# Performance work log

Measured on AMD Instinct MI355X. Metric: run time of the kernel, lower is better.

## Reference

```python
import jax, jax.numpy as jnp
import numpy as np

N_NODES = 50000
N_EDGES = 1600000
NODE_DIM = 1024
HID = 128
OUT = 128
LN_EPS = 1e-5


def setup_inputs() -> dict:
    key = jax.random.key(0)
    ks = jax.random.split(key, 8)
    s = lambda d: 1.0 / np.sqrt(d)
    return {
        "x": jax.random.normal(ks[0], (N_NODES, NODE_DIM), jnp.float32),
        "edge_index": jax.random.randint(ks[1], (2, N_EDGES), 0, N_NODES, jnp.int64),
        "proj_w": jax.random.normal(ks[2], (HID, NODE_DIM), jnp.float32) * s(NODE_DIM),
        "proj_b": jnp.zeros((HID,), jnp.float32),
        "lin_l_w": jax.random.normal(ks[3], (HID, HID), jnp.float32) * s(HID),
        "lin_l_b": jnp.zeros((HID,), jnp.float32),
        "lin_r_w": jax.random.normal(ks[4], (HID, HID), jnp.float32) * s(HID),
        "ln_g": jnp.ones((HID,), jnp.float32),
        "ln_b": jnp.zeros((HID,), jnp.float32),
        "out_w": jax.random.normal(ks[5], (OUT, HID), jnp.float32) * s(HID),
        "out_b": jnp.zeros((OUT,), jnp.float32),
    }


def reference(x, edge_index, proj_w, proj_b, lin_l_w, lin_l_b, lin_r_w, ln_g, ln_b, out_w, out_b):
    n = x.shape[0]
    # input projection + ReLU: [N, node_dim] -> [N, H]
    h = jax.nn.relu(x @ proj_w.T + proj_b)
    # SAGEConv(mean): gather source features, mean-scatter to targets
    src, dst = edge_index[0], edge_index[1]
    agg = jax.ops.segment_sum(h[src], dst, num_segments=n)  # [N, H]
    deg = jax.ops.segment_sum(jnp.ones((src.shape[0],), h.dtype), dst, num_segments=n)
    mean_nbr = agg / jnp.maximum(deg, 1.0)[:, None]
    h = mean_nbr @ lin_l_w.T + lin_l_b + h @ lin_r_w.T
    # LayerNorm over feature dim
    mu = h.mean(-1, keepdims=True)
    var = jnp.mean((h - mu) ** 2, -1, keepdims=True)
    h = (h - mu) * jax.lax.rsqrt(var + LN_EPS) * ln_g + ln_b
    h = jax.nn.relu(h)  # dropout is identity in eval
    # batch=None -> global mean pool over all nodes: [1, H]
    g = h.mean(0, keepdims=True)
    return g @ out_w.T + out_b
```

## Files before the change

### kernel.cpp

```cpp
#include <hip/hip_runtime.h>

#define N_NODES  50000
#define N_EDGES  1600000
#define NODE_DIM 1024
#define HID      128
#define LN_EPS   1e-5f
#define NBUCK    196
#define SHARD    6250

typedef float f32x4 __attribute__((ext_vector_type(4)));
typedef __bf16 bf16x8 __attribute__((ext_vector_type(8)));
typedef unsigned short u16x8 __attribute__((ext_vector_type(8)));

__device__ __forceinline__ unsigned short f2bf(float f) {
  __bf16 b = (__bf16)f;
  return __builtin_bit_cast(unsigned short, b);
}
__device__ __forceinline__ unsigned int pkbf(float a, float b) {
  return (unsigned int)f2bf(a) | ((unsigned int)f2bf(b) << 16);
}
__device__ __forceinline__ float bf2f(unsigned short v) {
  return __uint_as_float((unsigned int)v << 16);
}

__device__ __forceinline__ int scan256_excl(int v, int buf[2][256], int t) {
  int cur = 0;
  buf[0][t] = v;
  __syncthreads();
  for (int off = 1; off < 256; off <<= 1) {
    int nxt = cur ^ 1;
    int s = buf[cur][t];
    if (t >= off) s += buf[cur][t - off];
    buf[nxt][t] = s;
    cur = nxt;
    __syncthreads();
  }
  return buf[cur][t] - v;
}

__global__ __launch_bounds__(256) void k_wcvt(const float* __restrict__ w,
                                              unsigned short* __restrict__ wb) {
  int i = (blockIdx.x * 256 + threadIdx.x) * 4;
  float4 v = *(const float4*)(w + i);
  unsigned int* o = (unsigned int*)(wb + i);
  o[0] = pkbf(v.x, v.y);
  o[1] = pkbf(v.z, v.w);
}

#define LDR 40

__global__ __launch_bounds__(256) void k_proj(const float* __restrict__ x,
                                              const unsigned short* __restrict__ pwb,
                                              const float* __restrict__ pb,
                                              unsigned short* __restrict__ h) {
  __shared__ unsigned short As[2 * 64 * LDR];
  __shared__ unsigned short Bs[2 * 128 * LDR];
  const int tid = threadIdx.x;
  const int m0 = blockIdx.x * 64;
  const int wave = tid >> 6, lane = tid & 63;
  const int wm = (wave >> 1) * 32, wn = (wave & 1) * 64;
  const int fr = lane & 15, ko = (lane >> 4) * 8;

  const int arow = tid >> 2, akq = (tid & 3) * 16;
  const int grow = m0 + arow;
  const bool aval = (grow < N_NODES);
  const float* aptr = x + (size_t)grow * NODE_DIM + akq;
  const int brow = tid >> 1, bkq = (tid & 1) * 32;
  const unsigned short* bptr = pwb + (size_t)brow * NODE_DIM + bkq;

  f32x4 acc[2][4] = {};
  float4 av[4];
  u16x8 bv[4];

  auto LOAD = [&](int k0) {
    if (aval) {
      const float4* p = (const float4*)(aptr + k0);
#pragma unroll
      for (int j = 0; j < 4; j++) av[j] = p[j];
    } else {
#pragma unroll
      for (int j = 0; j < 4; j++) av[j] = make_float4(0.f, 0.f, 0.f, 0.f);
    }
    const u16x8* q = (const u16x8*)(bptr + k0);
#pragma unroll
    for (int j = 0; j < 4; j++) bv[j] = q[j];
  };

  LOAD(0);
  for (int k0 = 0; k0 < NODE_DIM; k0 += 64) {
    __syncthreads();
    unsigned int* da = (unsigned int*)&As[((akq >> 5) * 64 + arow) * LDR + (akq & 31)];
#pragma unroll
    for (int j = 0; j < 4; j++) {
      da[2 * j]     = pkbf(av[j].x, av[j].y);
      da[2 * j + 1] = pkbf(av[j].z, av[j].w);
    }
    u16x8* db = (u16x8*)&Bs[((bkq >> 5) * 128 + brow) * LDR];
#pragma unroll
    for (int j = 0; j < 4; j++) db[j] = bv[j];
    __syncthreads();

    if (k0 + 64 < NODE_DIM) LOAD(k0 + 64);

#pragma unroll
    for (int s = 0; s < 2; s++) {
      bf16x8 af[2], bfr[4];
#pragma unroll
      for (int m = 0; m < 2; m++)
        af[m] = *(const bf16x8*)&As[(s * 64 + wm + m * 16 + fr) * LDR + ko];
#pragma unroll
      for (int n = 0; n < 4; n++)
        bfr[n] = *(const bf16x8*)&Bs[(s * 128 + wn + n * 16 + fr) * LDR + ko];
#pragma unroll
      for (int m = 0; m < 2; m++)
#pragma unroll
        for (int n = 0; n < 4; n++)
          acc[m][n] = __builtin_amdgcn_mfma_f32_16x16x32_bf16(af[m], bfr[n], acc[m][n], 0, 0, 0);
    }
  }

  const int cr = (lane >> 4) * 4, cc = lane & 15;
#pragma unroll
  for (int n = 0; n < 4; n++) {
    const int col = wn + n * 16 + cc;
    const float bias = pb[col];
#pragma unroll
    for (int m = 0; m < 2; m++) {
#pragma unroll
      for (int i = 0; i < 4; i++) {
        const int row = m0 + wm + m * 16 + cr + i;
        if (row < N_NODES) {
          float v = acc[m][n][i] + bias;
          h[(size_t)row * HID + col] = f2bf(v > 0.f ? v : 0.f);
        }
      }
    }
  }
}

__global__ __launch_bounds__(256) void k_hist(const int* __restrict__ ei,
                                              int* __restrict__ counts) {
  __shared__ int bins[NBUCK];
  int t = threadIdx.x;
  if (t < NBUCK) bins[t] = 0;
  __syncthreads();
  int base = blockIdx.x * SHARD;
  for (int i = t; i < SHARD; i += 256)
    atomicAdd(&bins[ei[N_EDGES + base + i] >> 8], 1);
  __syncthreads();
  if (t < NBUCK) counts[t * 256 + blockIdx.x] = bins[t];
}

__global__ __launch_bounds__(256) void k_s1(const int* __restrict__ counts,
                                            int* __restrict__ basem,
                                            int* __restrict__ btot) {
  __shared__ int buf[2][256];
  int t = threadIdx.x, b = blockIdx.x;
  int v = counts[b * 256 + t];
  int excl = scan256_excl(v, buf, t);
  basem[b * 256 + t] = excl;
  if (t == 255) btot[b] = excl + v;
}

__global__ __launch_bounds__(256) void k_s2(const int* __restrict__ btot,
                                            int* __restrict__ bstart,
                                            float* __restrict__ accum) {
  __shared__ int buf[2][256];
  int t = threadIdx.x;
  int v = (t < NBUCK) ? btot[t] : 0;
  int excl = scan256_excl(v, buf, t);
  if (t < NBUCK) bstart[t] = excl;
  if (t == 0) bstart[NBUCK] = N_EDGES;
  if (t < HID) accum[t] = 0.f;
}

__global__ __launch_bounds__(256) void k_scatter(const int* __restrict__ ei,
                                                 const int* __restrict__ basem,
                                                 const int* __restrict__ bstart,
                                                 unsigned int* __restrict__ bs) {
  __shared__ int cur[NBUCK];
  int t = threadIdx.x;
  if (t < NBUCK) cur[t] = bstart[t] + basem[t * 256 + blockIdx.x];
  __syncthreads();
  int base = blockIdx.x * SHARD;
  for (int i = t; i < SHARD; i += 256) {
    int e = base + i;
    unsigned int src = (unsigned int)ei[e];
    unsigned int dst = (unsigned int)ei[N_EDGES + e];
    int pos = atomicAdd(&cur[dst >> 8], 1);
    bs[pos] = src | ((dst & 255u) << 16);
  }
}

__global__ __launch_bounds__(256) void k_bucket(const int* __restrict__ bstart,
                                                const unsigned int* __restrict__ bs,
                                                unsigned short* __restrict__ nbr,
                                                int* __restrict__ offs,
                                                int* __restrict__ deg) {
  __shared__ int bins[256];
  __shared__ int buf[2][256];
  __shared__ int curs[256];
  int t = threadIdx.x, b = blockIdx.x;
  int s = bstart[b], e = bstart[b + 1];
  bins[t] = 0;
  __syncthreads();
  for (int i = s + t; i < e; i += 256)
    atomicAdd(&bins[(bs[i] >> 16) & 255u], 1);
  __syncthreads();
  int v = bins[t];
  int excl = scan256_excl(v, buf, t);
  int node = b * 256 + t;
  deg[node]  = v;
  offs[node] = s + excl;
  curs[t]    = s + excl;
  __syncthreads();
  for (int i = s + t; i < e; i += 256) {
    unsigned int p = bs[i];
    int pos = atomicAdd(&curs[(p >> 16) & 255u], 1);
    nbr[pos] = (unsigned short)(p & 0xffffu);
  }
}

__global__ __launch_bounds__(256) void k_gather(const unsigned short* __restrict__ h,
                                                const unsigned short* __restrict__ nbr,
                                                const int* __restrict__ offs,
                                                const int* __restrict__ deg,
                                                unsigned short* __restrict__ mn) {
  const int wave = threadIdx.x >> 6;
  const int lane = threadIdx.x & 63;
  const int node = blockIdx.x * 4 + wave;
  if (node >= N_NODES) return;
  const int g = lane >> 4, li = lane & 15;
  const int d  = deg[node];
  const int st = offs[node];
  float a[8] = {0.f, 0.f, 0.f, 0.f, 0.f, 0.f, 0.f, 0.f};
  int n = g;
  for (; n + 4 < d; n += 8) {
    int s0 = nbr[st + n];
    int s1 = nbr[st + n + 4];
    u16x8 v0 = *(const u16x8*)(h + (size_t)s0 * HID + li * 8);
    u16x8 v1 = *(const u16x8*)(h + (size_t)s1 * HID + li * 8);
#pragma unroll
    for (int k = 0; k < 8; k++) a[k] += bf2f(v0[k]) + bf2f(v1[k]);
  }
  if (n < d) {
    int s0 = nbr[st + n];
    u16x8 v0 = *(const u16x8*)(h + (size_t)s0 * HID + li * 8);
#pragma unroll
    for (int k = 0; k < 8; k++) a[k] += bf2f(v0[k]);
  }
#pragma unroll
  for (int k = 0; k < 8; k++) {
    a[k] += __shfl_xor(a[k], 16);
    a[k] += __shfl_xor(a[k], 32);
  }
  if (g == 0) {
    float inv = 1.f / fmaxf((float)d, 1.f);
    u16x8 r;
#pragma unroll
    for (int k = 0; k < 8; k++) r[k] = f2bf(a[k] * inv);
    *(u16x8*)(mn + (size_t)node * HID + li * 8) = r;
  }
}

__global__ __launch_bounds__(256) void k_sage(const unsigned short* __restrict__ mn,
                                              const unsigned short* __restrict__ h,
                                              const float* __restrict__ wl,
                                              const float* __restrict__ wr,
                                              const float* __restrict__ lb,
                                              const float* __restrict__ lg,
                                              const float* __restrict__ lbt,
                                              float* __restrict__ accum) {
  __shared__ unsigned short As[128 * 32];
  __shared__ unsigned short Bs[128 * 32];
  __shared__ float T3[32 * 128];
  __shared__ float red[4][128];
  const int tid = threadIdx.x;
  const int m0 = blockIdx.x * 128;
  const int wave = tid >> 6, lane = tid & 63;
  const int wm = (wave >> 1) * 64, wn = (wave & 1) * 64;
  const int srow = tid >> 1, scol = (tid & 1) * 16;
  const int fr = lane & 15, ko = (lane >> 4) * 8;

  f32x4 acc[4][4] = {};

  for (int k0 = 0; k0 < 2 * HID; k0 += 32) {
    const unsigned short* baseA = (k0 < HID) ? mn : h;
    const float* baseB = (k0 < HID) ? wl : wr;
    const int kk = (k0 & (HID - 1)) + scol;
    const int arow = m0 + srow;
    u16x8 a0 = {0, 0, 0, 0, 0, 0, 0, 0}, a1 = a0;
    if (arow < N_NODES) {
      const u16x8* p = (const u16x8*)(baseA + (size_t)arow * HID + kk);
      a0 = p[0]; a1 = p[1];
    }
    const float4* q = (const float4*)(baseB + (size_t)srow * HID + kk);
    float4 b0 = q[0], b1 = q[1], b2 = q[2], b3 = q[3];

    __syncthreads();
    *(u16x8*)&As[srow * 32 + scol]     = a0;
    *(u16x8*)&As[srow * 32 + scol + 8] = a1;
    unsigned int* db = (unsigned int*)&Bs[srow * 32 + scol];
    db[0] = pkbf(b0.x, b0.y); db[1] = pkbf(b0.z, b0.w);
    db[2] = pkbf(b1.x, b1.y); db[3] = pkbf(b1.z, b1.w);
    db[4] = pkbf(b2.x, b2.y); db[5] = pkbf(b2.z, b2.w);
    db[6] = pkbf(b3.x, b3.y); db[7] = pkbf(b3.z, b3.w);
    __syncthreads();

    bf16x8 af[4], bfr[4];
#pragma unroll
    for (int m = 0; m < 4; m++)
      af[m] = *(const bf16x8*)&As[(wm + m * 16 + fr) * 32 + ko];
#pragma unroll
    for (int n = 0; n < 4; n++)
      bfr[n] = *(const bf16x8*)&Bs[(wn + n * 16 + fr) * 32 + ko];
#pragma unroll
    for (int m = 0; m < 4; m++)
#pragma unroll
      for (int n = 0; n < 4; n++)
        acc[m][n] = __builtin_amdgcn_mfma_f32_16x16x32_bf16(af[m], bfr[n], acc[m][n], 0, 0, 0);
  }

  const int cr = (lane >> 4) * 4, cc = lane & 15;
  const int p = wave >> 1;
  const float g0 = lg[lane], g1 = lg[lane + 64];
  const float t0 = lbt[lane], t1 = lbt[lane + 64];
  float ax = 0.f, ay = 0.f;
#pragma unroll
  for (int m = 0; m < 4; m++) {
    __syncthreads();
#pragma unroll
    for (int n = 0; n < 4; n++) {
      const int col = wn + n * 16 + cc;
      const float bias = lb[col];
#pragma unroll
      for (int i = 0; i < 4; i++)
        T3[(p * 16 + cr + i) * 128 + col] = acc[m][n][i] + bias;
    }
    __syncthreads();
    for (int r8 = 0; r8 < 8; r8++) {
      int q8 = wave * 8 + r8;
      int grow = m0 + (q8 >> 4) * 64 + m * 16 + (q8 & 15);
      float v0 = T3[q8 * 128 + lane];
      float v1 = T3[q8 * 128 + lane + 64];
      float sum = v0 + v1, ss = v0 * v0 + v1 * v1;
#pragma unroll
      for (int off = 32; off > 0; off >>= 1) {
        sum += __shfl_xor(sum, off);
        ss  += __shfl_xor(ss, off);
      }
      float mu  = sum * (1.f / HID);
      float var = ss * (1.f / HID) - mu * mu;
      float rinv = rsqrtf(var + LN_EPS);
      if (grow < N_NODES) {
        float y0 = (v0 - mu) * rinv * g0 + t0;
        float y1 = (v1 - mu) * rinv * g1 + t1;
        ax += fmaxf(y0, 0.f);
        ay += fmaxf(y1, 0.f);
      }
    }
  }
  red[wave][lane]      = ax;
  red[wave][lane + 64] = ay;
  __syncthreads();
  if (wave == 0) {
    float a  = red[0][lane] + red[1][lane] + red[2][lane] + red[3][lane];
    float bb = red[0][lane + 64] + red[1][lane + 64] + red[2][lane + 64] + red[3][lane + 64];
    atomicAdd(&accum[lane], a);
    atomicAdd(&accum[lane + 64], bb);
  }
}

__global__ __launch_bounds__(128) void k_final(const float* __restrict__ accum,
                                               const float* __restrict__ ow,
                                               const float* __restrict__ ob,
                                               float* __restrict__ out) {
  __shared__ float gs[HID];
  int t = threadIdx.x;
  gs[t] = accum[t] * (1.f / N_NODES);
  __syncthreads();
  float s = ob[t];
  for (int k = 0; k < HID; k++) s += gs[k] * ow[t * HID + k];
  out[t] = s;
}

extern "C" void kernel_launch(void* const* d_in, const int* in_sizes, int n_in,
                              void* d_out, int out_size, void* d_ws, size_t ws_size,
                              hipStream_t stream) {
  const float* x   = (const float*)d_in[0];
  const int*   ei  = (const int*)d_in[1];
  const float* pw  = (const float*)d_in[2];
  const float* pb  = (const float*)d_in[3];
  const float* wl  = (const float*)d_in[4];
  const float* lb  = (const float*)d_in[5];
  const float* wr  = (const float*)d_in[6];
  const float* lg  = (const float*)d_in[7];
  const float* lbt = (const float*)d_in[8];
  const float* ow  = (const float*)d_in[9];
  const float* ob  = (const float*)d_in[10];
  float* out = (float*)d_out;

  const int PAD = NBUCK * 256;
  unsigned short* h  = (unsigned short*)d_ws;
  unsigned short* mn = h + (size_t)PAD * HID;
  unsigned int* bsp  = (unsigned int*)(mn + (size_t)PAD * HID);
  unsigned short* nbr = (unsigned short*)(bsp + N_EDGES);
  int* counts = (int*)(nbr + N_EDGES);
  int* basem  = counts + NBUCK * 256;
  int* btot   = basem + NBUCK * 256;
  int* bstart = btot + 256;
  int* offs   = bstart + 256;
  int* deg    = offs + PAD;
  float* accum = (float*)(deg + PAD);
  unsigned short* pwb = (unsigned short*)(accum + 128);

  const int MB  = (N_NODES + 127) / 128;
  const int MB2 = (N_NODES + 63) / 64;

  hipLaunchKernelGGL(k_wcvt,    dim3(HID * NODE_DIM / 1024), dim3(256), 0, stream, pw, pwb);
  hipLaunchKernelGGL(k_proj,    dim3(MB2),   dim3(256), 0, stream, x, pwb, pb, h);
  hipLaunchKernelGGL(k_hist,    dim3(256),   dim3(256), 0, stream, ei, counts);
  hipLaunchKernelGGL(k_s1,      dim3(NBUCK), dim3(256), 0, stream, counts, basem, btot);
  hipLaunchKernelGGL(k_s2,      dim3(1),     dim3(256), 0, stream, btot, bstart, accum);
  hipLaunchKernelGGL(k_scatter, dim3(256),   dim3(256), 0, stream, ei, basem, bstart, bsp);
  hipLaunchKernelGGL(k_bucket,  dim3(NBUCK), dim3(256), 0, stream, bstart, bsp, nbr, offs, deg);
  hipLaunchKernelGGL(k_gather,  dim3((N_NODES + 3) / 4), dim3(256), 0, stream, h, nbr, offs, deg, mn);
  hipLaunchKernelGGL(k_sage,    dim3(MB),    dim3(256), 0, stream, mn, h, wl, wr, lb, lg, lbt, accum);
  hipLaunchKernelGGL(k_final,   dim3(1),     dim3(128), 0, stream, accum, ow, ob, out);
}
```

Baseline: 475.6 us.

## Widen projection GEMM K-tile to 128 with XOR-swizzled LDS and coalesced loads

```diff
diff --git a/kernel.cpp b/kernel.cpp
--- a/kernel.cpp
+++ b/kernel.cpp
@@ -47,70 +47,79 @@
   o[1] = pkbf(v.z, v.w);
 }
 
-#define LDR 40
-
-__global__ __launch_bounds__(256) void k_proj(const float* __restrict__ x,
-                                              const unsigned short* __restrict__ pwb,
-                                              const float* __restrict__ pb,
-                                              unsigned short* __restrict__ h) {
-  __shared__ unsigned short As[2 * 64 * LDR];
-  __shared__ unsigned short Bs[2 * 128 * LDR];
+__global__ __launch_bounds__(256, 3) void k_proj(const float* __restrict__ x,
+                                                 const unsigned short* __restrict__ pwb,
+                                                 const float* __restrict__ pb,
+                                                 unsigned short* __restrict__ h) {
+  __shared__ unsigned short As[64 * 128];
+  __shared__ unsigned short Bs[128 * 128];
   const int tid = threadIdx.x;
   const int m0 = blockIdx.x * 64;
   const int wave = tid >> 6, lane = tid & 63;
   const int wm = (wave >> 1) * 32, wn = (wave & 1) * 64;
-  const int fr = lane & 15, ko = (lane >> 4) * 8;
-
-  const int arow = tid >> 2, akq = (tid & 3) * 16;
-  const int grow = m0 + arow;
-  const bool aval = (grow < N_NODES);
-  const float* aptr = x + (size_t)grow * NODE_DIM + akq;
-  const int brow = tid >> 1, bkq = (tid & 1) * 32;
-  const unsigned short* bptr = pwb + (size_t)brow * NODE_DIM + bkq;
+  const int fr = lane & 15;
+
+  const int arL = wave * 16 + (lane >> 5);
+  const int acF = (lane & 31) * 4;
+  const int brL = wave * 32 + (lane >> 4);
+  const int bcE = (lane & 15) * 8;
 
   f32x4 acc[2][4] = {};
-  float4 av[4];
-  u16x8 bv[4];
+  float4 av[8];
+  u16x8 bv[8];
 
   auto LOAD = [&](int k0) {
-    if (aval) {
-      const float4* p = (const float4*)(aptr + k0);
-#pragma unroll
-      for (int j = 0; j < 4; j++) av[j] = p[j];
-    } else {
-#pragma unroll
-      for (int j = 0; j < 4; j++) av[j] = make_float4(0.f, 0.f, 0.f, 0.f);
-    }
-    const u16x8* q = (const u16x8*)(bptr + k0);
-#pragma unroll
-    for (int j = 0; j < 4; j++) bv[j] = q[j];
+#pragma unroll
+    for (int j = 0; j < 8; j++) {
+      const int r = arL + j * 2;
+      const int grow = m0 + r;
+      if (grow < N_NODES)
+        av[j] = *(const float4*)(x + (size_t)grow * NODE_DIM + k0 + acF);
+      else
+        av[j] = make_float4(0.f, 0.f, 0.f, 0.f);
+    }
+#pragma unroll
+    for (int j = 0; j < 8; j++) {
+      const int r = brL + j * 4;
+      bv[j] = *(const u16x8*)(pwb + (size_t)r * NODE_DIM + k0 + bcE);
+    }
   };
 
   LOAD(0);
-  for (int k0 = 0; k0 < NODE_DIM; k0 += 64) {
-    __syncthreads();
-    unsigned int* da = (unsigned int*)&As[((akq >> 5) * 64 + arow) * LDR + (akq & 31)];
-#pragma unroll
-    for (int j = 0; j < 4; j++) {
-      da[2 * j]     = pkbf(av[j].x, av[j].y);
-      da[2 * j + 1] = pkbf(av[j].z, av[j].w);
-    }
-    u16x8* db = (u16x8*)&Bs[((bkq >> 5) * 128 + brow) * LDR];
-#pragma unroll
-    for (int j = 0; j < 4; j++) db[j] = bv[j];
-    __syncthreads();
-
-    if (k0 + 64 < NODE_DIM) LOAD(k0 + 64);
-
-#pragma unroll
-    for (int s = 0; s < 2; s++) {
+  for (int k0 = 0; k0 < NODE_DIM; k0 += 128) {
+    __syncthreads();
+#pragma unroll
+    for (int j = 0; j < 8; j++) {
+      const int r = arL + j * 2;
+      const int off = r * 256 + (((lane & 31) * 8) ^ ((r & 7) << 4));
+      unsigned int lo = pkbf(av[j].x, av[j].y);
+      unsigned int hi = pkbf(av[j].z, av[j].w);
+      *(uint2*)((char*)As + off) = make_uint2(lo, hi);
+    }
+#pragma unroll
+    for (int j = 0; j < 8; j++) {
+      const int r = brL + j * 4;
+      const int off = r * 256 + (((lane & 15) * 16) ^ ((r & 7) << 4));
+      *(u16x8*)((char*)Bs + off) = bv[j];
+    }
+    __syncthreads();
+
+    if (k0 + 128 < NODE_DIM) LOAD(k0 + 128);
+
+#pragma unroll
+    for (int s = 0; s < 4; s++) {
+      const int kb = s * 64 + (lane >> 4) * 16;
       bf16x8 af[2], bfr[4];
 #pragma unroll
-      for (int m = 0; m < 2; m++)
-        af[m] = *(const bf16x8*)&As[(s * 64 + wm + m * 16 + fr) * LDR + ko];
-#pragma unroll
-      for (int n = 0; n < 4; n++)
-        bfr[n] = *(const bf16x8*)&Bs[(s * 128 + wn + n * 16 + fr) * LDR + ko];
+      for (int m = 0; m < 2; m++) {
+        const int r = wm + m * 16 + fr;
+        af[m] = *(const bf16x8*)((char*)As + r * 256 + (kb ^ ((r & 7) << 4)));
+      }
+#pragma unroll
+      for (int n = 0; n < 4; n++) {
+        const int r = wn + n * 16 + fr;
+        bfr[n] = *(const bf16x8*)((char*)Bs + r * 256 + (kb ^ ((r & 7) << 4)));
+      }
 #pragma unroll
       for (int m = 0; m < 2; m++)
 #pragma unroll
```

After: 470.9 us. No clear change (-1.0%).
